# Kernel optimization log

Measured on AMD Instinct MI355X. Metric: run time of the kernel, lower is better.

## Reference

```python
import jax, jax.numpy as jnp
import numpy as np

B, N, K, C = 8, 4096, 32, 64
RADIUS = 0.15
CIN = C + 3  # dp_fj: concat(dp[3], fj[C])


def _ball_query(p, radius, k):
    """p: (B,N,3). Returns neighbor indices (B,N,K): first k points (in index
    order) within radius of each query, padded with the first valid neighbor
    (ballquery semantics; query point itself is always index 0 candidate)."""
    sq = jnp.sum(p * p, axis=-1)                                  # (B,N)
    d2 = sq[:, :, None] + sq[:, None, :] - 2.0 * jnp.einsum('bnd,bmd->bnm', p, p)
    n = p.shape[1]
    within = d2 <= radius * radius
    key = jnp.where(within, jnp.arange(n, dtype=jnp.int32)[None, None, :], n)
    order = jnp.argsort(key, axis=-1)[..., :k]                    # (B,N,K)
    valid = jnp.take_along_axis(key, order, axis=-1) < n
    first = order[..., :1]
    return jnp.where(valid, order, first)


def _conv2d_1x1(x, w, b):
    # x: (B,Cin,N,K), w: (Cout,Cin), b: (Cout,)
    return jnp.einsum('oi,bink->bonk', w, x) + b[None, :, None, None]


def _conv1d_1x1(x, w, b):
    # x: (B,Cin,N)
    return jnp.einsum('oi,bin->bon', w, x) + b[None, :, None]


def setup_inputs() -> dict:
    key = jax.random.key(0)
    ks = jax.random.split(key, 16)
    s = 0.05
    inp = {
        'p': jax.random.uniform(ks[0], (B, N, 3), dtype=jnp.float32),
        'f': jax.random.normal(ks[1], (B, C, N), dtype=jnp.float32),
        # attn_local: convblock2d (CIN -> C), no act
        'w_attn': jax.random.normal(ks[2], (C, CIN), dtype=jnp.float32) * s,
        'b_attn': jnp.zeros((C,), jnp.float32),
        # convs: convblock2d (CIN -> C, relu) then (C -> C, no act)
        'w1': jax.random.normal(ks[3], (C, CIN), dtype=jnp.float32) * s,
        'b1': jnp.zeros((C,), jnp.float32),
        'w2': jax.random.normal(ks[4], (C, C), dtype=jnp.float32) * s,
        'b2': jnp.zeros((C,), jnp.float32),
        # ffn: convblock1d (C -> C*expansion=C, relu) then (C -> C, no act)
        'wf1': jax.random.normal(ks[5], (C, C), dtype=jnp.float32) * s,
        'bf1': jnp.zeros((C,), jnp.float32),
        'wf2': jax.random.normal(ks[6], (C, C), dtype=jnp.float32) * s,
        'bf2': jnp.zeros((C,), jnp.float32),
    }
    return inp


def reference(p, f, w_attn, b_attn, w1, b1, w2, b2, wf1, bf1, wf2, bf2):
    bidx = jnp.arange(B)[:, None, None]
    idx = _ball_query(p, RADIUS, K)                               # (B,N,K) int
    pj = p[bidx, idx]                                             # (B,N,K,3)
    dp = (pj - p[:, :, None, :]).transpose(0, 3, 1, 2)            # (B,3,N,K)
    ft = f.transpose(0, 2, 1)                                     # (B,N,C)
    fj = ft[bidx, idx].transpose(0, 3, 1, 2)                      # (B,C,N,K)

    fj_cat = jnp.concatenate([dp, fj], axis=1)                    # (B,CIN,N,K)

    attn = _conv2d_1x1(fj_cat, w_attn, b_attn)                    # (B,C,N,K)
    x = jax.nn.relu(_conv2d_1x1(fj_cat, w1, b1))
    x = _conv2d_1x1(x, w2, b2)                                    # (B,C,N,K)

    # new_attention, 4D path: softmax over neighbor axis (tau=1), weighted sum
    channel_attn = jax.nn.softmax(attn, axis=-1)
    fout = jnp.sum(channel_attn * x, axis=-1)                     # (B,C,N)

    fout = jax.nn.relu(fout + f)
    identity = fout
    h = jax.nn.relu(_conv1d_1x1(fout, wf1, bf1))
    h = _conv1d_1x1(h, wf2, bf2)
    fout = jax.nn.relu(h + identity)                              # use_res
    return (p, fout)
```

## Files before the change

### kernel.cpp

```cpp
#include <hip/hip_runtime.h>

#define B_ 8
#define N_ 4096
#define K_ 32
#define C_ 64
#define CIN_ 67
#define R2_ 0.0225f

#define NCELL 6
#define CELLS 216
#define HCAP 160

#define SFJ 104
#define SY1 72
#define SFB 72
#define PTS 4
#define ITERS 4

typedef short short8v __attribute__((ext_vector_type(8)));
typedef short short4v __attribute__((ext_vector_type(4)));
typedef float floatx4 __attribute__((ext_vector_type(4)));

__device__ __forceinline__ short f2bf(float x) {
    unsigned u = __float_as_uint(x);
    u += 0x7fffu + ((u >> 16) & 1u);
    return (short)(u >> 16);
}

template <int CTRL>
__device__ __forceinline__ float dpp_add(float x) {
    const int m = __builtin_amdgcn_update_dpp(0, __float_as_int(x), CTRL, 0xF, 0xF, false);
    return x + __int_as_float(m);
}
__device__ __forceinline__ float row16_sum(float x) {
    x = dpp_add<0xB1>(x);
    x = dpp_add<0x4E>(x);
    x = dpp_add<0x141>(x);
    x = dpp_add<0x140>(x);
    return x;
}

__global__ __launch_bounds__(256) void prep_kernel(
    const float* __restrict__ p, const float* __restrict__ f,
    unsigned short* __restrict__ ftb, float4* __restrict__ p4,
    float* __restrict__ pout, int* __restrict__ cell_start,
    float4* __restrict__ sp4, unsigned short* __restrict__ sidx)
{
#pragma clang fp contract(off)
    __shared__ __align__(16) short tile[64 * 72];
    __shared__ int s_scan[256];
    __shared__ int s_cur[CELLS];
    const int t = threadIdx.x;
    const int b = blockIdx.x >> 6;
    const int n0 = (blockIdx.x & 63) * 64;
    const int nn4 = t & 15, ch = t >> 4;
    for (int cc = 0; cc < 4; ++cc) {
        const int c = cc * 16 + ch;
        const float4 v = *(const float4*)&f[((size_t)(b * 64 + c)) * N_ + n0 + nn4 * 4];
        tile[(nn4 * 4 + 0) * 72 + c] = f2bf(v.x);
        tile[(nn4 * 4 + 1) * 72 + c] = f2bf(v.y);
        tile[(nn4 * 4 + 2) * 72 + c] = f2bf(v.z);
        tile[(nn4 * 4 + 3) * 72 + c] = f2bf(v.w);
    }
    if (t < 48) {
        const size_t base = ((size_t)(b * N_ + n0)) * 3;
        ((float4*)(pout + base))[t] = ((const float4*)(p + base))[t];
    }
    if (t < 64) {
        const int n = n0 + t;
        const float x = p[((size_t)(b * N_ + n)) * 3 + 0];
        const float y = p[((size_t)(b * N_ + n)) * 3 + 1];
        const float z = p[((size_t)(b * N_ + n)) * 3 + 2];
        const float sq = (x * x + y * y) + z * z;
        p4[(size_t)b * N_ + n] = make_float4(x, y, z, sq);
    }
    __syncthreads();
    {
        const int nn = t >> 2, cb = (t & 3) * 16;
        uint4* dst = (uint4*)&ftb[((size_t)(b * N_ + n0 + nn)) * 64 + cb];
        const uint4* src = (const uint4*)&tile[nn * 72 + cb];
        dst[0] = src[0];
        dst[1] = src[1];
    }

    if ((blockIdx.x & 63) == 0) {
        unsigned short* cellof = (unsigned short*)tile;
        const float* pb = p + (size_t)b * N_ * 3;
        __syncthreads();
        if (t < CELLS) s_cur[t] = 0;
        __syncthreads();
        for (int n = t; n < N_; n += 256) {
            const int cx = min((int)(pb[n * 3 + 0] * 6.0f), 5);
            const int cy = min((int)(pb[n * 3 + 1] * 6.0f), 5);
            const int cz = min((int)(pb[n * 3 + 2] * 6.0f), 5);
            const int c = (cx * 6 + cy) * 6 + cz;
            cellof[n] = (unsigned short)c;
            atomicAdd(&s_cur[c], 1);
        }
        __syncthreads();
        s_scan[t] = (t < CELLS) ? s_cur[t] : 0;
        __syncthreads();
        #pragma unroll
        for (int off = 1; off < 256; off <<= 1) {
            int x = s_scan[t];
            if (t >= off) x += s_scan[t - off];
            __syncthreads();
            s_scan[t] = x;
            __syncthreads();
        }
        const int excl = (t == 0) ? 0 : s_scan[t - 1];
        if (t < CELLS + 1) cell_start[b * (CELLS + 1) + t] = excl;
        if (t < CELLS) s_cur[t] = excl;
        __syncthreads();
        for (int n = t; n < N_; n += 256) {
            const int c = cellof[n];
            const int pos = atomicAdd(&s_cur[c], 1);
            const float x = pb[n * 3 + 0], y = pb[n * 3 + 1], z = pb[n * 3 + 2];
            const float sq = (x * x + y * y) + z * z;
            sp4[(size_t)b * N_ + pos] = make_float4(x, y, z, sq);
            sidx[(size_t)b * N_ + pos] = (unsigned short)n;
        }
    }
}

__global__ __launch_bounds__(256) void ball_query_grid_kernel(
    const float4* __restrict__ p4, const float4* __restrict__ sp4,
    const unsigned short* __restrict__ sidx, const int* __restrict__ cell_start,
    unsigned short* __restrict__ idx)
{
#pragma clang fp contract(off)
    __shared__ unsigned short s_hits[4][HCAP];
    const int lane = threadIdx.x & 63;
    const int w = threadIdx.x >> 6;
    const int q = blockIdx.x * 4 + w;
    const int b = q >> 12;
    const int n = q & (N_ - 1);
    const float4 Q = p4[(size_t)b * N_ + n];
    const int cx = min((int)(Q.x * 6.0f), 5);
    const int cy = min((int)(Q.y * 6.0f), 5);
    const int cz = min((int)(Q.z * 6.0f), 5);
    const int* cs = cell_start + b * (CELLS + 1);
    const float4* sp = sp4 + (size_t)b * N_;
    const unsigned short* si = sidx + (size_t)b * N_;

    const int x0 = max(cx - 1, 0), x1 = min(cx + 1, 5);
    const int y0 = max(cy - 1, 0), y1 = min(cy + 1, 5);
    const int z0 = max(cz - 1, 0), z1 = min(cz + 1, 5);
    const unsigned long long below = (1ull << lane) - 1ull;

    int H = 0;
    for (int xx = x0; xx <= x1; ++xx)
    for (int yy = y0; yy <= y1; ++yy) {
        const int rbase = (xx * 6 + yy) * 6;
        const int beg = cs[rbase + z0];
        const int end = cs[rbase + z1 + 1];
        for (int s = beg; s < end; s += 64) {
            const int i = s + lane;
            bool hit = false;
            unsigned short oi = 0;
            if (i < end) {
                const float4 A = sp[i];
                const float d2 = (Q.w + A.w)
                    - 2.0f * ((Q.x * A.x + Q.y * A.y) + Q.z * A.z);
                hit = (d2 <= R2_);
                oi = si[i];
            }
            const unsigned long long m = __ballot(hit);
            if (hit) {
                const int pos = H + __popcll(m & below);
                if (pos < HCAP) s_hits[w][pos] = oi;
            }
            H += __popcll(m);
        }
    }
    if (H > HCAP) H = HCAP;

    unsigned short* o = idx + (size_t)q * K_;
    if (H <= K_) {
        int v = (lane < H) ? (int)s_hits[w][lane] : 0x7FFFFFFF;
        for (int d = 32; d; d >>= 1) v = min(v, __shfl_xor(v, d));
        if (lane < K_)
            o[lane] = (lane < H) ? s_hits[w][lane] : (unsigned short)v;
    } else {
        const int h0 = (lane       < H) ? (int)s_hits[w][lane      ] : 0x7FFF;
        const int h1 = (lane + 64  < H) ? (int)s_hits[w][lane + 64 ] : 0x7FFF;
        const int h2 = (lane + 128 < H) ? (int)s_hits[w][lane + 128] : 0x7FFF;
        int lo = 0, hi = N_ - 1;
        while (lo < hi) {
            const int mid = (lo + hi) >> 1;
            int c = (h0 <= mid) + (h1 <= mid) + (h2 <= mid);
            for (int d = 32; d; d >>= 1) c += __shfl_xor(c, d);
            if (c >= K_) hi = mid; else lo = mid + 1;
        }
        const unsigned long long m0 = __ballot(h0 <= lo);
        if (h0 <= lo) o[__popcll(m0 & below)] = (unsigned short)h0;
        int base = __popcll(m0);
        const unsigned long long m1 = __ballot(h1 <= lo);
        if (h1 <= lo) o[base + __popcll(m1 & below)] = (unsigned short)h1;
        base += __popcll(m1);
        const unsigned long long m2 = __ballot(h2 <= lo);
        if (h2 <= lo) o[base + __popcll(m2 & below)] = (unsigned short)h2;
    }
}

__global__ __launch_bounds__(256, 3) void lpa_mfma_kernel(
    const float4* __restrict__ p4, const float* __restrict__ f,
    const unsigned short* __restrict__ ftb,
    const float* __restrict__ w_attn, const float* __restrict__ b_attn,
    const float* __restrict__ w1, const float* __restrict__ b1,
    const float* __restrict__ w2, const float* __restrict__ b2,
    const float* __restrict__ wf1, const float* __restrict__ bf1,
    const float* __restrict__ wf2, const float* __restrict__ bf2,
    const unsigned short* __restrict__ idx, float* __restrict__ out)
{
    __shared__ __align__(16) short s_fj[128 * SFJ];
    __shared__ __align__(16) short s_y1[128 * SY1];
    __shared__ __align__(16) short s_fbuf[2 * 16 * SFB];
    __shared__ float s_vec[PTS * 64];
    short* s_vecbf = s_fbuf;
    short* s_hbf   = s_fbuf + 16 * SFB;

    const int t = threadIdx.x;
    const int lane = t & 63;
    const int mb = t >> 6;
    const int l15 = lane & 15;
    const int quad = lane >> 4;

    short8v wa_f[3], w1_f[3], w2_f[2], wf1_f[2], wf2_f[2];
    {
        const int cm = mb * 16 + l15;
        #pragma unroll
        for (int ks = 0; ks < 3; ++ks) {
            short8v a, bq;
            #pragma unroll
            for (int j = 0; j < 8; ++j) {
                const int ip = ks * 32 + quad * 8 + j;
                float va = 0.0f, vb = 0.0f;
                if (ip < 64)      { va = w_attn[cm * CIN_ + ip + 3];  vb = w1[cm * CIN_ + ip + 3]; }
                else if (ip < 67) { va = w_attn[cm * CIN_ + ip - 64]; vb = w1[cm * CIN_ + ip - 64]; }
                a[j] = f2bf(va); bq[j] = f2bf(vb);
            }
            wa_f[ks] = a; w1_f[ks] = bq;
        }
        #pragma unroll
        for (int ks = 0; ks < 2; ++ks) {
            short8v a, bq, cq;
            #pragma unroll
            for (int j = 0; j < 8; ++j) {
                const int kk = ks * 32 + quad * 8 + j;
                a[j]  = f2bf(w2[cm * 64 + kk]);
                bq[j] = f2bf(wf1[cm * 64 + kk]);
                cq[j] = f2bf(wf2[cm * 64 + kk]);
            }
            w2_f[ks] = a; wf1_f[ks] = bq; wf2_f[ks] = cq;
        }
    }

    const int crow = mb * 16 + quad * 4;
    const float4 bav  = *(const float4*)&b_attn[crow];
    const float4 b1v  = *(const float4*)&b1[crow];
    const float4 b2v  = *(const float4*)&b2[crow];
    const float4 bf1v = *(const float4*)&bf1[crow];
    const float4 bf2v = *(const float4*)&bf2[crow];

    for (int e = t; e < 512; e += 256) {
        const int col = e >> 2, c4 = e & 3;
        *(uint4*)&s_fj[col * SFJ + 72 + c4 * 8] = make_uint4(0u, 0u, 0u, 0u);
    }
    for (int e = t; e < 1152; e += 256) ((unsigned*)s_fbuf)[e] = 0u;

    const int pt00 = blockIdx.x * (PTS * ITERS);
    const int bb = pt00 >> 12;
    const float4* pb = p4 + (size_t)bb * N_;

    for (int itn = 0; itn < ITERS; ++itn) {
        const int pt0 = pt00 + itn * PTS;

        {
            const int col = t >> 1, h = t & 1;
            const int j = idx[(size_t)pt0 * K_ + col];
            const uint4* src = (const uint4*)&ftb[((size_t)(bb * N_ + j)) * 64 + h * 32];
            uint4* dst = (uint4*)&s_fj[col * SFJ + h * 32];
            dst[0] = src[0]; dst[1] = src[1]; dst[2] = src[2]; dst[3] = src[3];
            if (h) {
                const int n = (pt0 + (col >> 5)) & (N_ - 1);
                const float4 Pj = pb[j];
                const float4 Pn = pb[n];
                short8v dp = {};
                dp[0] = f2bf(Pj.x - Pn.x);
                dp[1] = f2bf(Pj.y - Pn.y);
                dp[2] = f2bf(Pj.z - Pn.z);
                *(short8v*)&s_fj[col * SFJ + 64] = dp;
            }
        }
        __syncthreads();

        floatx4 accA[8];
        #pragma unroll
        for (int nt = 0; nt < 8; ++nt) {
            const short* bp = &s_fj[(nt * 16 + l15) * SFJ + quad * 8];
            const short8v fb0 = *(const short8v*)(bp);
            const short8v fb1 = *(const short8v*)(bp + 32);
            const short8v fb2 = *(const short8v*)(bp + 64);
            floatx4 a = {0.f, 0.f, 0.f, 0.f};
            a = __builtin_amdgcn_mfma_f32_16x16x32_bf16(wa_f[0], fb0, a, 0, 0, 0);
            a = __builtin_amdgcn_mfma_f32_16x16x32_bf16(wa_f[1], fb1, a, 0, 0, 0);
            a = __builtin_amdgcn_mfma_f32_16x16x32_bf16(wa_f[2], fb2, a, 0, 0, 0);
            accA[nt] = a;
            floatx4 y = {0.f, 0.f, 0.f, 0.f};
            y = __builtin_amdgcn_mfma_f32_16x16x32_bf16(w1_f[0], fb0, y, 0, 0, 0);
            y = __builtin_amdgcn_mfma_f32_16x16x32_bf16(w1_f[1], fb1, y, 0, 0, 0);
            y = __builtin_amdgcn_mfma_f32_16x16x32_bf16(w1_f[2], fb2, y, 0, 0, 0);
            short4v yp;
            yp[0] = f2bf(fmaxf(y[0] + b1v.x, 0.f));
            yp[1] = f2bf(fmaxf(y[1] + b1v.y, 0.f));
            yp[2] = f2bf(fmaxf(y[2] + b1v.z, 0.f));
            yp[3] = f2bf(fmaxf(y[3] + b1v.w, 0.f));
            *(short4v*)&s_y1[(nt * 16 + l15) * SY1 + crow] = yp;
        }
        __syncthreads();

        floatx4 accX[8];
        #pragma unroll
        for (int nt = 0; nt < 8; ++nt) {
            const short* bp = &s_y1[(nt * 16 + l15) * SY1 + quad * 8];
            const short8v yb0 = *(const short8v*)(bp);
            const short8v yb1 = *(const short8v*)(bp + 32);
            floatx4 x = {0.f, 0.f, 0.f, 0.f};
            x = __builtin_amdgcn_mfma_f32_16x16x32_bf16(w2_f[0], yb0, x, 0, 0, 0);
            x = __builtin_amdgcn_mfma_f32_16x16x32_bf16(w2_f[1], yb1, x, 0, 0, 0);
            accX[nt] = x;
        }

        #pragma unroll
        for (int pi = 0; pi < PTS; ++pi) {
            const int n = (pt0 + pi) & (N_ - 1);
            float fo[4];
            #pragma unroll
            for (int r = 0; r < 4; ++r) {
                const float ba = (r == 0) ? bav.x : (r == 1) ? bav.y : (r == 2) ? bav.z : bav.w;
                const float bx = (r == 0) ? b2v.x : (r == 1) ? b2v.y : (r == 2) ? b2v.z : b2v.w;
                const float e0 = __expf(accA[2 * pi][r] + ba);
                const float e1 = __expf(accA[2 * pi + 1][r] + ba);
                const float se = row16_sum(e0 + e1);
                const float sw = row16_sum(e0 * (accX[2 * pi][r] + bx)
                                         + e1 * (accX[2 * pi + 1][r] + bx));
                const float fres = f[((size_t)(bb * 64 + crow + r)) * N_ + n];
                fo[r] = fmaxf(sw * __builtin_amdgcn_rcpf(se) + fres, 0.f);
            }
            if (l15 == 0) {
                *(float4*)&s_vec[pi * 64 + crow] = make_float4(fo[0], fo[1], fo[2], fo[3]);
                short4v fb;
                fb[0] = f2bf(fo[0]); fb[1] = f2bf(fo[1]);
                fb[2] = f2bf(fo[2]); fb[3] = f2bf(fo[3]);
                *(short4v*)&s_vecbf[pi * SFB + crow] = fb;
            }
        }
        __syncthreads();

        {
            const short8v vb0 = *(const short8v*)&s_vecbf[l15 * SFB + quad * 8];
            const short8v vb1 = *(const short8v*)&s_vecbf[l15 * SFB + 32 + quad * 8];
            floatx4 d = {0.f, 0.f, 0.f, 0.f};
            d = __builtin_amdgcn_mfma_f32_16x16x32_bf16(wf1_f[0], vb0, d, 0, 0, 0);
            d = __builtin_amdgcn_mfma_f32_16x16x32_bf16(wf1_f[1], vb1, d, 0, 0, 0);
            if (l15 < PTS) {
                short4v hb;
                hb[0] = f2bf(fmaxf(d[0] + bf1v.x, 0.f));
                hb[1] = f2bf(fmaxf(d[1] + bf1v.y, 0.f));
                hb[2] = f2bf(fmaxf(d[2] + bf1v.z, 0.f));
                hb[3] = f2bf(fmaxf(d[3] + bf1v.w, 0.f));
                *(short4v*)&s_hbf[l15 * SFB + crow] = hb;
            }
        }
        __syncthreads();

        {
            const short8v hb0 = *(const short8v*)&s_hbf[l15 * SFB + quad * 8];
            const short8v hb1 = *(const short8v*)&s_hbf[l15 * SFB + 32 + quad * 8];
            floatx4 d = {0.f, 0.f, 0.f, 0.f};
            d = __builtin_amdgcn_mfma_f32_16x16x32_bf16(wf2_f[0], hb0, d, 0, 0, 0);
            d = __builtin_amdgcn_mfma_f32_16x16x32_bf16(wf2_f[1], hb1, d, 0, 0, 0);
            if (l15 < PTS) {
                const int n = (pt0 + l15) & (N_ - 1);
                out[((size_t)(bb * 64 + crow + 0)) * N_ + n] =
                    fmaxf(d[0] + bf2v.x + s_vec[l15 * 64 + crow + 0], 0.f);
                out[((size_t)(bb * 64 + crow + 1)) * N_ + n] =
                    fmaxf(d[1] + bf2v.y + s_vec[l15 * 64 + crow + 1], 0.f);
                out[((size_t)(bb * 64 + crow + 2)) * N_ + n] =
                    fmaxf(d[2] + bf2v.z + s_vec[l15 * 64 + crow + 2], 0.f);
                out[((size_t)(bb * 64 + crow + 3)) * N_ + n] =
                    fmaxf(d[3] + bf2v.w + s_vec[l15 * 64 + crow + 3], 0.f);
            }
        }
    }
}

extern "C" void kernel_launch(void* const* d_in, const int* in_sizes, int n_in,
                              void* d_out, int out_size, void* d_ws, size_t ws_size,
                              hipStream_t stream)
{
    const float* p      = (const float*)d_in[0];
    const float* f      = (const float*)d_in[1];
    const float* w_attn = (const float*)d_in[2];
    const float* b_attn = (const float*)d_in[3];
    const float* w1     = (const float*)d_in[4];
    const float* b1     = (const float*)d_in[5];
    const float* w2     = (const float*)d_in[6];
    const float* b2     = (const float*)d_in[7];
    const float* wf1    = (const float*)d_in[8];
    const float* bf1    = (const float*)d_in[9];
    const float* wf2    = (const float*)d_in[10];
    const float* bf2    = (const float*)d_in[11];
    float* out = (float*)d_out;

    char* ws = (char*)d_ws;
    unsigned short* ftb  = (unsigned short*)(ws);
    float4* p4           = (float4*)(ws + 4194304);
    float4* sp4          = (float4*)(ws + 4718592);
    unsigned short* sidx = (unsigned short*)(ws + 5242880);
    int* cell_start      = (int*)(ws + 5308416);
    unsigned short* idx  = (unsigned short*)(ws + 5315584);

    prep_kernel<<<B_ * (N_ / 64), 256, 0, stream>>>(
        p, f, ftb, p4, out, cell_start, sp4, sidx);
    ball_query_grid_kernel<<<(B_ * N_) / 4, 256, 0, stream>>>(
        p4, sp4, sidx, cell_start, idx);
    lpa_mfma_kernel<<<(B_ * N_) / (PTS * ITERS), 256, 0, stream>>>(
        p4, f, ftb, w_attn, b_attn, w1, b1, w2, b2, wf1, bf1, wf2, bf2,
        idx, out + (size_t)B_ * N_ * 3);
}
```

Measured before the change: 236.7 us.

## Fuse grid ball query into the MFMA attention kernel via shared-memory indices

Removes the separate ball-query kernel launch and computes neighbor indices for the block's 16 query points at the start of the main MFMA kernel. Each wave handles 4 queries and writes the indices to a shared-memory array instead of a global idx buffer. This drops one kernel launch and the global write/read round trip of the index array. In exchange it adds shared memory (with a possible occupancy risk at launch_bounds 3), and the ball-query phase now runs serially before the compute loop inside each block, so its latency is exposed there rather than spread across its own grid.

Result: slower. 269.5 us (+13.9%).

```diff
diff --git a/kernel.cpp b/kernel.cpp
--- a/kernel.cpp
+++ b/kernel.cpp
@@ -123,100 +123,24 @@
     }
 }
 
-__global__ __launch_bounds__(256) void ball_query_grid_kernel(
-    const float4* __restrict__ p4, const float4* __restrict__ sp4,
-    const unsigned short* __restrict__ sidx, const int* __restrict__ cell_start,
-    unsigned short* __restrict__ idx)
-{
-#pragma clang fp contract(off)
-    __shared__ unsigned short s_hits[4][HCAP];
-    const int lane = threadIdx.x & 63;
-    const int w = threadIdx.x >> 6;
-    const int q = blockIdx.x * 4 + w;
-    const int b = q >> 12;
-    const int n = q & (N_ - 1);
-    const float4 Q = p4[(size_t)b * N_ + n];
-    const int cx = min((int)(Q.x * 6.0f), 5);
-    const int cy = min((int)(Q.y * 6.0f), 5);
-    const int cz = min((int)(Q.z * 6.0f), 5);
-    const int* cs = cell_start + b * (CELLS + 1);
-    const float4* sp = sp4 + (size_t)b * N_;
-    const unsigned short* si = sidx + (size_t)b * N_;
-
-    const int x0 = max(cx - 1, 0), x1 = min(cx + 1, 5);
-    const int y0 = max(cy - 1, 0), y1 = min(cy + 1, 5);
-    const int z0 = max(cz - 1, 0), z1 = min(cz + 1, 5);
-    const unsigned long long below = (1ull << lane) - 1ull;
-
-    int H = 0;
-    for (int xx = x0; xx <= x1; ++xx)
-    for (int yy = y0; yy <= y1; ++yy) {
-        const int rbase = (xx * 6 + yy) * 6;
-        const int beg = cs[rbase + z0];
-        const int end = cs[rbase + z1 + 1];
-        for (int s = beg; s < end; s += 64) {
-            const int i = s + lane;
-            bool hit = false;
-            unsigned short oi = 0;
-            if (i < end) {
-                const float4 A = sp[i];
-                const float d2 = (Q.w + A.w)
-                    - 2.0f * ((Q.x * A.x + Q.y * A.y) + Q.z * A.z);
-                hit = (d2 <= R2_);
-                oi = si[i];
-            }
-            const unsigned long long m = __ballot(hit);
-            if (hit) {
-                const int pos = H + __popcll(m & below);
-                if (pos < HCAP) s_hits[w][pos] = oi;
-            }
-            H += __popcll(m);
-        }
-    }
-    if (H > HCAP) H = HCAP;
-
-    unsigned short* o = idx + (size_t)q * K_;
-    if (H <= K_) {
-        int v = (lane < H) ? (int)s_hits[w][lane] : 0x7FFFFFFF;
-        for (int d = 32; d; d >>= 1) v = min(v, __shfl_xor(v, d));
-        if (lane < K_)
-            o[lane] = (lane < H) ? s_hits[w][lane] : (unsigned short)v;
-    } else {
-        const int h0 = (lane       < H) ? (int)s_hits[w][lane      ] : 0x7FFF;
-        const int h1 = (lane + 64  < H) ? (int)s_hits[w][lane + 64 ] : 0x7FFF;
-        const int h2 = (lane + 128 < H) ? (int)s_hits[w][lane + 128] : 0x7FFF;
-        int lo = 0, hi = N_ - 1;
-        while (lo < hi) {
-            const int mid = (lo + hi) >> 1;
-            int c = (h0 <= mid) + (h1 <= mid) + (h2 <= mid);
-            for (int d = 32; d; d >>= 1) c += __shfl_xor(c, d);
-            if (c >= K_) hi = mid; else lo = mid + 1;
-        }
-        const unsigned long long m0 = __ballot(h0 <= lo);
-        if (h0 <= lo) o[__popcll(m0 & below)] = (unsigned short)h0;
-        int base = __popcll(m0);
-        const unsigned long long m1 = __ballot(h1 <= lo);
-        if (h1 <= lo) o[base + __popcll(m1 & below)] = (unsigned short)h1;
-        base += __popcll(m1);
-        const unsigned long long m2 = __ballot(h2 <= lo);
-        if (h2 <= lo) o[base + __popcll(m2 & below)] = (unsigned short)h2;
-    }
-}
-
 __global__ __launch_bounds__(256, 3) void lpa_mfma_kernel(
     const float4* __restrict__ p4, const float* __restrict__ f,
     const unsigned short* __restrict__ ftb,
+    const float4* __restrict__ sp4, const unsigned short* __restrict__ sidx,
+    const int* __restrict__ cell_start,
     const float* __restrict__ w_attn, const float* __restrict__ b_attn,
     const float* __restrict__ w1, const float* __restrict__ b1,
     const float* __restrict__ w2, const float* __restrict__ b2,
     const float* __restrict__ wf1, const float* __restrict__ bf1,
     const float* __restrict__ wf2, const float* __restrict__ bf2,
-    const unsigned short* __restrict__ idx, float* __restrict__ out)
+    float* __restrict__ out)
 {
     __shared__ __align__(16) short s_fj[128 * SFJ];
     __shared__ __align__(16) short s_y1[128 * SY1];
     __shared__ __align__(16) short s_fbuf[2 * 16 * SFB];
     __shared__ float s_vec[PTS * 64];
+    __shared__ unsigned short s_idx[16 * K_];
+    __shared__ unsigned short s_hits[4][HCAP];
     short* s_vecbf = s_fbuf;
     short* s_hbf   = s_fbuf + 16 * SFB;
 
@@ -225,6 +149,83 @@
     const int mb = t >> 6;
     const int l15 = lane & 15;
     const int quad = lane >> 4;
+
+    const int pt00 = blockIdx.x * (PTS * ITERS);
+    const int bb = pt00 >> 12;
+    const float4* pb = p4 + (size_t)bb * N_;
+
+    {
+#pragma clang fp contract(off)
+        const int* cs = cell_start + bb * (CELLS + 1);
+        const float4* sp = sp4 + (size_t)bb * N_;
+        const unsigned short* si = sidx + (size_t)bb * N_;
+        const unsigned long long below = (1ull << lane) - 1ull;
+        for (int qq = 0; qq < 4; ++qq) {
+            const int qi = mb * 4 + qq;
+            const int n = (pt00 + qi) & (N_ - 1);
+            const float4 Q = pb[n];
+            const int cx = min((int)(Q.x * 6.0f), 5);
+            const int cy = min((int)(Q.y * 6.0f), 5);
+            const int cz = min((int)(Q.z * 6.0f), 5);
+            const int x0 = max(cx - 1, 0), x1 = min(cx + 1, 5);
+            const int y0 = max(cy - 1, 0), y1 = min(cy + 1, 5);
+            const int z0 = max(cz - 1, 0), z1 = min(cz + 1, 5);
+
+            int H = 0;
+            for (int xx = x0; xx <= x1; ++xx)
+            for (int yy = y0; yy <= y1; ++yy) {
+                const int rbase = (xx * 6 + yy) * 6;
+                const int beg = cs[rbase + z0];
+                const int end = cs[rbase + z1 + 1];
+                for (int s = beg; s < end; s += 64) {
+                    const int i = s + lane;
+                    bool hit = false;
+                    unsigned short oi = 0;
+                    if (i < end) {
+                        const float4 A = sp[i];
+                        const float d2 = (Q.w + A.w)
+                            - 2.0f * ((Q.x * A.x + Q.y * A.y) + Q.z * A.z);
+                        hit = (d2 <= R2_);
+                        oi = si[i];
+                    }
+                    const unsigned long long m = __ballot(hit);
+                    if (hit) {
+                        const int pos = H + __popcll(m & below);
+                        if (pos < HCAP) s_hits[mb][pos] = oi;
+                    }
+                    H += __popcll(m);
+                }
+            }
+            if (H > HCAP) H = HCAP;
+
+            unsigned short* o = &s_idx[qi * K_];
+            if (H <= K_) {
+                int v = (lane < H) ? (int)s_hits[mb][lane] : 0x7FFFFFFF;
+                for (int d = 32; d; d >>= 1) v = min(v, __shfl_xor(v, d));
+                if (lane < K_)
+                    o[lane] = (lane < H) ? s_hits[mb][lane] : (unsigned short)v;
+            } else {
+                const int h0 = (lane       < H) ? (int)s_hits[mb][lane      ] : 0x7FFF;
+                const int h1 = (lane + 64  < H) ? (int)s_hits[mb][lane + 64 ] : 0x7FFF;
+                const int h2 = (lane + 128 < H) ? (int)s_hits[mb][lane + 128] : 0x7FFF;
+                int lo = 0, hi = N_ - 1;
+                while (lo < hi) {
+                    const int mid = (lo + hi) >> 1;
+                    int c = (h0 <= mid) + (h1 <= mid) + (h2 <= mid);
+                    for (int d = 32; d; d >>= 1) c += __shfl_xor(c, d);
+                    if (c >= K_) hi = mid; else lo = mid + 1;
+                }
+                const unsigned long long m0 = __ballot(h0 <= lo);
+                if (h0 <= lo) o[__popcll(m0 & below)] = (unsigned short)h0;
+                int base = __popcll(m0);
+                const unsigned long long m1 = __ballot(h1 <= lo);
+                if (h1 <= lo) o[base + __popcll(m1 & below)] = (unsigned short)h1;
+                base += __popcll(m1);
+                const unsigned long long m2 = __ballot(h2 <= lo);
+                if (h2 <= lo) o[base + __popcll(m2 & below)] = (unsigned short)h2;
+            }
+        }
+    }
 
     short8v wa_f[3], w1_f[3], w2_f[2], wf1_f[2], wf2_f[2];
     {
@@ -269,16 +270,14 @@
     }
     for (int e = t; e < 1152; e += 256) ((unsigned*)s_fbuf)[e] = 0u;
 
-    const int pt00 = blockIdx.x * (PTS * ITERS);
-    const int bb = pt00 >> 12;
-    const float4* pb = p4 + (size_t)bb * N_;
+    __syncthreads();
 
     for (int itn = 0; itn < ITERS; ++itn) {
         const int pt0 = pt00 + itn * PTS;
 
         {
             const int col = t >> 1, h = t & 1;
-            const int j = idx[(size_t)pt0 * K_ + col];
+            const int j = s_idx[itn * 128 + col];
             const uint4* src = (const uint4*)&ftb[((size_t)(bb * N_ + j)) * 64 + h * 32];
             uint4* dst = (uint4*)&s_fj[col * SFJ + h * 32];
             dst[0] = src[0]; dst[1] = src[1]; dst[2] = src[2]; dst[3] = src[3];
@@ -420,13 +419,11 @@
     float4* sp4          = (float4*)(ws + 4718592);
     unsigned short* sidx = (unsigned short*)(ws + 5242880);
     int* cell_start      = (int*)(ws + 5308416);
-    unsigned short* idx  = (unsigned short*)(ws + 5315584);
 
     prep_kernel<<<B_ * (N_ / 64), 256, 0, stream>>>(
         p, f, ftb, p4, out, cell_start, sp4, sidx);
-    ball_query_grid_kernel<<<(B_ * N_) / 4, 256, 0, stream>>>(
-        p4, sp4, sidx, cell_start, idx);
     lpa_mfma_kernel<<<(B_ * N_) / (PTS * ITERS), 256, 0, stream>>>(
-        p4, f, ftb, w_attn, b_attn, w1, b1, w2, b2, wf1, bf1, wf2, bf2,
-        idx, out + (size_t)B_ * N_ * 3);
-}
+        p4, f, ftb, sp4, sidx, cell_start,
+        w_attn, b_attn, w1, b1, w2, b2, wf1, bf1, wf2, bf2,
+        out + (size_t)B_ * N_ * 3);
+}
```
